# Optimization experiments

Measured on AMD Instinct MI355X. Metric: run time of the kernel, lower is better.

## Reference

```python
import jax, jax.numpy as jnp
import numpy as np

N_HEADS = 16
HEAD_DIM = 128
ROPE_BASE = 50000.0
EPS = 1e-06


def _rotate_half(x):
    half = x.shape[-1] // 2
    return jnp.concatenate([-x[..., half:], x[..., :half]], axis=-1)


def _rms_norm(x, w):
    rms = jnp.sqrt(jnp.mean(x * x, axis=-1, keepdims=True) + EPS)
    return w * (x / rms)


def _rope_tables(n, dim, dtype):
    inv_freq = 1.0 / (ROPE_BASE ** (jnp.arange(0, dim, 2, dtype=jnp.float32) / dim))
    t = jnp.arange(n, dtype=jnp.float32)
    freqs = jnp.outer(t, inv_freq)          # [n, dim/2]
    emb = jnp.concatenate([freqs, freqs], axis=-1)  # [n, dim]
    return jnp.cos(emb).astype(dtype), jnp.sin(emb).astype(dtype)


def setup_inputs() -> dict:
    key = jax.random.key(0)
    ks = jax.random.split(key, 5)
    B, n, d = 2, 2048, 2048
    inner = N_HEADS * HEAD_DIM
    s = 1.0 / np.sqrt(d)
    return {
        "x": jax.random.normal(ks[0], (B, n, d), jnp.float32),
        "Wq": jax.random.normal(ks[1], (d, inner), jnp.float32) * s,
        "Wk": jax.random.normal(ks[2], (d, inner), jnp.float32) * s,
        "Wv": jax.random.normal(ks[3], (d, inner), jnp.float32) * s,
        "Wo": jax.random.normal(ks[4], (inner, d), jnp.float32) * s,
        "qn_w": jnp.ones((inner,), jnp.float32),
        "kn_w": jnp.ones((inner,), jnp.float32),
    }


def reference(x, Wq, Wk, Wv, Wo, qn_w, kn_w):
    B, n, d = x.shape
    # QKV projections (no bias)
    q = x @ Wq
    k = x @ Wk
    v = x @ Wv
    # QK RMSNorm over full inner_dim (as in the torch module)
    q = _rms_norm(q, qn_w)
    k = _rms_norm(k, kn_w)
    # [B, H, n, Dh]
    q = q.reshape(B, n, N_HEADS, HEAD_DIM).transpose(0, 2, 1, 3)
    k = k.reshape(B, n, N_HEADS, HEAD_DIM).transpose(0, 2, 1, 3)
    v = v.reshape(B, n, N_HEADS, HEAD_DIM).transpose(0, 2, 1, 3)
    # RoPE (rotary_dim == head_dim -> full rotation)
    cos, sin = _rope_tables(n, HEAD_DIM, x.dtype)  # [n, Dh]
    cos = cos[None, None]
    sin = sin[None, None]
    q = q * cos + _rotate_half(q) * sin
    k = k * cos + _rotate_half(k) * sin
    # Causal SDPA
    scale = 1.0 / np.sqrt(HEAD_DIM)
    scores = jnp.einsum("bhqd,bhkd->bhqk", q, k) * scale
    causal = jnp.tril(jnp.ones((n, n), dtype=bool))
    scores = jnp.where(causal, scores, jnp.finfo(scores.dtype).min)
    attn = jax.nn.softmax(scores, axis=-1)
    out = jnp.einsum("bhqk,bhkd->bhqd", attn, v)
    out = out.transpose(0, 2, 1, 3).reshape(B, n, N_HEADS * HEAD_DIM)
    return out @ Wo
```

## Files before the change

### kernel.cpp

```cpp
#include <hip/hip_runtime.h>

typedef unsigned short u16;
typedef unsigned int u32;
typedef __attribute__((ext_vector_type(8))) short short8;
typedef __attribute__((ext_vector_type(4))) float f32x4;

typedef __attribute__((address_space(3))) unsigned int as3u32;
typedef __attribute__((address_space(1))) unsigned int as1u32;

__device__ __forceinline__ void gld16(void* lds, const void* g) {
    __builtin_amdgcn_global_load_lds((as1u32*)(void*)g, (as3u32*)lds, 16, 0, 0);
}

__device__ inline float bf2f(u16 u) {
    u32 v = ((u32)u) << 16;
    return __builtin_bit_cast(float, v);
}
__device__ inline u16 f2bf(float f) {
    u32 u = __builtin_bit_cast(u32, f);
    u32 r = u + 0x7FFF + ((u >> 16) & 1);
    return (u16)(r >> 16);
}
__device__ inline void unpack8(uint4 v, float* f) {
    u32 a[4] = {v.x, v.y, v.z, v.w};
#pragma unroll
    for (int i = 0; i < 4; ++i) {
        f[2 * i]     = bf2f((u16)(a[i] & 0xffff));
        f[2 * i + 1] = bf2f((u16)(a[i] >> 16));
    }
}

__global__ __launch_bounds__(256) void cast_f32_bf16(const float* __restrict__ in,
                                                     u16* __restrict__ out, int n) {
    int i = (blockIdx.x * 256 + threadIdx.x) * 4;
    if (i >= n) return;
    float4 v = *(const float4*)&in[i];
    ushort4 o;
    o.x = f2bf(v.x); o.y = f2bf(v.y); o.z = f2bf(v.z); o.w = f2bf(v.w);
    *(ushort4*)&out[i] = o;
}

__global__ __launch_bounds__(256) void transpose_cast(const float* __restrict__ in,
                                                      u16* __restrict__ out, int dim) {
    __shared__ float tile[32][33];
    const int n0 = blockIdx.x * 32, k0 = blockIdx.y * 32;
    const int tx = threadIdx.x & 31, ty = threadIdx.x >> 5;
#pragma unroll
    for (int i = 0; i < 32; i += 8)
        tile[ty + i][tx] = in[(size_t)(k0 + ty + i) * dim + n0 + tx];
    __syncthreads();
#pragma unroll
    for (int i = 0; i < 32; i += 8)
        out[(size_t)(n0 + ty + i) * dim + k0 + tx] = f2bf(tile[tx][ty + i]);
}

__global__ __launch_bounds__(256) void rope_tables(float* __restrict__ cosb,
                                                   float* __restrict__ sinb) {
    int idx = blockIdx.x * 256 + threadIdx.x;
    int pos = idx >> 6, i = idx & 63;
    float invf = __expf(-(float)i * (10.819778284410283f / 64.0f));
    float a = (float)pos * invf;
    cosb[idx] = cosf(a);
    sinb[idx] = sinf(a);
}

template <bool BF16OUT>
__global__ __launch_bounds__(256) void gemm_bt(const u16* __restrict__ A,
                                               const u16* __restrict__ Bt,
                                               void* __restrict__ Cv,
                                               int M, int N, int K) {
    __shared__ u16 As[128][64];
    __shared__ u16 Bs[128][64];
    const int bm = blockIdx.y, bn = blockIdx.x;
    const int tid = threadIdx.x;
    const int lane = tid & 63, w = tid >> 6;
    const int wm = (w >> 1) * 64, wn = (w & 1) * 64;
    const int lrow = lane & 15;
    const int sw = (lane & 7) << 4;
    const int srl = lane >> 3;
    const int ssw = ((lane & 7) * 16) ^ (srl << 4);
    const char* AB = (const char*)A;
    const char* BB = (const char*)Bt;
    f32x4 acc[4][4] = {};

    for (int k0 = 0; k0 < K; k0 += 64) {
        __syncthreads();
#pragma unroll
        for (int i = 0; i < 4; ++i) {
            const int rb = i * 32 + w * 8;
            gld16(&As[rb][0], AB + ((size_t)(bm * 128 + rb + srl) * K + k0) * 2 + ssw);
            gld16(&Bs[rb][0], BB + ((size_t)(bn * 128 + rb + srl) * K + k0) * 2 + ssw);
        }
        __syncthreads();
        const char* AsB = (const char*)As;
        const char* BsB = (const char*)Bs;
#pragma unroll
        for (int kk = 0; kk < 2; ++kk) {
            const int cb = (kk * 64 + (lane >> 4) * 16) ^ sw;
            short8 af[4], bf_[4];
#pragma unroll
            for (int i = 0; i < 4; ++i)
                af[i] = *(const short8*)(AsB + (wm + i * 16 + lrow) * 128 + cb);
#pragma unroll
            for (int j = 0; j < 4; ++j)
                bf_[j] = *(const short8*)(BsB + (wn + j * 16 + lrow) * 128 + cb);
#pragma unroll
            for (int i = 0; i < 4; ++i)
#pragma unroll
                for (int j = 0; j < 4; ++j)
                    acc[i][j] = __builtin_amdgcn_mfma_f32_16x16x32_bf16(af[i], bf_[j], acc[i][j], 0, 0, 0);
        }
    }
    const int crow = (lane >> 4) * 4, ccol = lane & 15;
#pragma unroll
    for (int i = 0; i < 4; ++i)
#pragma unroll
        for (int j = 0; j < 4; ++j)
#pragma unroll
            for (int r = 0; r < 4; ++r) {
                size_t off = (size_t)(bm * 128 + wm + i * 16 + crow + r) * N +
                             (size_t)(bn * 128 + wn + j * 16 + ccol);
                if (BF16OUT) ((u16*)Cv)[off] = f2bf(acc[i][j][r]);
                else         ((float*)Cv)[off] = acc[i][j][r];
            }
}

__global__ __launch_bounds__(256) void norm_rope(const u16* __restrict__ qkv,
                                                 const float* __restrict__ qw,
                                                 const float* __restrict__ kw,
                                                 const float* __restrict__ cosb,
                                                 const float* __restrict__ sinb,
                                                 u16* __restrict__ Qout,
                                                 u16* __restrict__ Kout) {
    __shared__ float qf[2048];
    __shared__ float kf[2048];
    __shared__ float red[8];
    const int r = blockIdx.x;
    const int b = r >> 11, pos = r & 2047;
    const int t = threadIdx.x;
    const u16* row = qkv + (size_t)r * 6144;
    uint4 qv = *(const uint4*)&row[t * 8];
    uint4 kv = *(const uint4*)&row[2048 + t * 8];
    float qe[8], ke[8];
    unpack8(qv, qe);
    unpack8(kv, ke);
    float sq = 0.f, sk = 0.f;
#pragma unroll
    for (int e = 0; e < 8; ++e) {
        qf[t * 8 + e] = qe[e];
        kf[t * 8 + e] = ke[e];
        sq += qe[e] * qe[e];
        sk += ke[e] * ke[e];
    }
#pragma unroll
    for (int msk = 1; msk < 64; msk <<= 1) {
        sq += __shfl_xor(sq, msk);
        sk += __shfl_xor(sk, msk);
    }
    if ((t & 63) == 0) { red[t >> 6] = sq; red[4 + (t >> 6)] = sk; }
    __syncthreads();
    float ssq = red[0] + red[1] + red[2] + red[3];
    float ssk = red[4] + red[5] + red[6] + red[7];
    const float invq = 0.12751946f / sqrtf(ssq * (1.f / 2048.f) + 1e-6f);
    const float invk = 1.0f / sqrtf(ssk * (1.f / 2048.f) + 1e-6f);
    const float* ct = cosb + pos * 64;
    const float* st = sinb + pos * 64;
    u16 qo[8], ko[8];
#pragma unroll
    for (int e = 0; e < 8; ++e) {
        int c = t * 8 + e;
        int jl = c & 127;
        int hb = c & ~127;
        int jj = jl & 63;
        float cs = ct[jj], sn = st[jj];
        int pair = hb + ((jl < 64) ? jl + 64 : jl - 64);
        float sgn = (jl < 64) ? -1.f : 1.f;
        float xq = qf[c] * qw[c], pq = qf[pair] * qw[pair];
        float xk = kf[c] * kw[c], pk = kf[pair] * kw[pair];
        qo[e] = f2bf((xq * cs + sgn * pq * sn) * invq);
        ko[e] = f2bf((xk * cs + sgn * pk * sn) * invk);
    }
    const int h = (t * 8) >> 7;
    const int j0 = (t * 8) & 127;
    size_t o = ((size_t)(b * 16 + h) * 2048 + pos) * 128 + j0;
    *(uint4*)&Qout[o] = *(uint4*)qo;
    *(uint4*)&Kout[o] = *(uint4*)ko;
}

__global__ __launch_bounds__(256) void v_transpose(const u16* __restrict__ qkv,
                                                   u16* __restrict__ Vt) {
    __shared__ u16 tile[64][40];
    const int bxx = blockIdx.x;
    const int jt = bxx & 3, pt = (bxx >> 2) & 31, bh = bxx >> 7;
    const int b = bh >> 4, h = bh & 15;
    const int pos0 = pt * 64, j0 = jt * 32;
    const int t = threadIdx.x;
    {
        int p = t >> 2, jc = (t & 3) * 8;
        const u16* src = qkv + (size_t)(b * 2048 + pos0 + p) * 6144 + 4096 + h * 128 + j0 + jc;
        *(uint4*)&tile[p][jc] = *(const uint4*)src;
    }
    __syncthreads();
    {
        int j = t >> 3, pc = (t & 7) * 8;
        u16 tmp[8];
#pragma unroll
        for (int e = 0; e < 8; ++e) tmp[e] = tile[pc + e][j];
        *(uint4*)&Vt[((size_t)bh * 128 + j0 + j) * 2048 + pos0 + pc] = *(uint4*)tmp;
    }
}

__global__ __launch_bounds__(256) void attn_fwd(const u16* __restrict__ Qr,
                                                const u16* __restrict__ Kr,
                                                const u16* __restrict__ Vt,
                                                u16* __restrict__ O) {
    __shared__ u16 Ks[2][64][128];
    __shared__ u16 Vs[2][128][64];
    __shared__ u16 Pb[4][16][68];
    const int bx = blockIdx.x;
    const int bh = bx >> 4, pi = bx & 15;
    const int tid = threadIdx.x;
    const int lane = tid & 63, w = tid >> 6;
    const int lrow = lane & 15, lk8 = (lane >> 4) * 8;
    const int sw = (lane & 7) << 4;
    const char* KhB = (const char*)(Kr + (size_t)bh * 2048 * 128);
    const char* VhB = (const char*)(Vt + (size_t)bh * 128 * 2048);
    const u16* Qh = Qr + (size_t)bh * 2048 * 128;
    const int b = bh >> 4, h = bh & 15;
    const int krl = lane >> 4;
    const int ksc = (lane & 15) * 16;
    const int vrl = lane >> 3;
    const int vsc = (lane & 7) * 16;

    short8 vone;
#pragma unroll
    for (int i = 0; i < 8; ++i) vone[i] = (short)0x3F80;

    for (int half = 0; half < 2; ++half) {
        const int qt = half ? (31 - pi) : pi;
        const int q0w = qt * 64 + w * 16;
        short8 qa[4];
#pragma unroll
        for (int d = 0; d < 4; ++d)
            qa[d] = *(const short8*)&Qh[(size_t)(q0w + lrow) * 128 + d * 32 + lk8];

        f32x4 acc[9] = {};
        float m[4] = {-3e38f, -3e38f, -3e38f, -3e38f};
        const int rbase = q0w + (lane >> 4) * 4;
        const int kend = qt * 64 + 64;

        __syncthreads();
#pragma unroll
        for (int j = 0; j < 4; ++j) {
            const int krb = w * 16 + j * 4;
            const int kr = krb + krl;
            gld16(&Ks[0][krb][0], KhB + (size_t)kr * 256 + (ksc ^ ((kr & 7) << 4)));
            const int vrb = w * 32 + j * 8;
            const int vr = vrb + vrl;
            gld16(&Vs[0][vrb][0], VhB + (size_t)vr * 4096 + (vsc ^ ((vr & 7) << 4)));
        }

        for (int k0 = 0; k0 < kend; k0 += 64) {
            const int buf = (k0 >> 6) & 1;
            __syncthreads();
            if (k0 + 64 < kend) {
                const int kn = k0 + 64;
#pragma unroll
                for (int j = 0; j < 4; ++j) {
                    const int krb = w * 16 + j * 4;
                    const int kr = krb + krl;
                    gld16(&Ks[buf ^ 1][krb][0],
                          KhB + (size_t)(kn + kr) * 256 + (ksc ^ ((kr & 7) << 4)));
                    const int vrb = w * 32 + j * 8;
                    const int vr = vrb + vrl;
                    gld16(&Vs[buf ^ 1][vrb][0],
                          VhB + (size_t)vr * 4096 + (size_t)kn * 2 + (vsc ^ ((vr & 7) << 4)));
                }
            }
            const char* KsB = (const char*)&Ks[buf][0][0];
            const char* VsB = (const char*)&Vs[buf][0][0];

            f32x4 s[4] = {};
            __builtin_amdgcn_s_setprio(1);
#pragma unroll
            for (int j = 0; j < 4; ++j)
#pragma unroll
                for (int d = 0; d < 4; ++d) {
                    short8 kb = *(const short8*)(KsB + (j * 16 + lrow) * 256 +
                                                 ((d * 64 + (lane >> 4) * 16) ^ sw));
                    s[j] = __builtin_amdgcn_mfma_f32_16x16x32_bf16(qa[d], kb, s[j], 0, 0, 0);
                }
            __builtin_amdgcn_s_setprio(0);

            const bool last = (k0 + 64 >= kend);
            float mx[4];
#pragma unroll
            for (int r = 0; r < 4; ++r) {
                const int rowg = rbase + r;
                if (last) {
#pragma unroll
                    for (int j = 0; j < 4; ++j) {
                        int c = k0 + j * 16 + lrow;
                        s[j][r] = (c <= rowg) ? s[j][r] : -1e30f;
                    }
                }
                float v0 = fmaxf(s[0][r], s[1][r]);
                float v1 = fmaxf(s[2][r], s[3][r]);
                float mr = fmaxf(v0, v1);
#pragma unroll
                for (int msk = 1; msk < 16; msk <<= 1) mr = fmaxf(mr, __shfl_xor(mr, msk));
                mx[r] = mr;
            }
            const bool need = (mx[0] > m[0] + 8.f) | (mx[1] > m[1] + 8.f) |
                              (mx[2] > m[2] + 8.f) | (mx[3] > m[3] + 8.f);
            if (__any(need)) {
                float corr[4];
#pragma unroll
                for (int r = 0; r < 4; ++r) {
                    float mn = fmaxf(m[r], mx[r]);
                    corr[r] = exp2f(m[r] - mn);
                    m[r] = mn;
                }
#pragma unroll
                for (int dt = 0; dt < 9; ++dt) {
                    f32x4 tv = acc[dt];
                    tv[0] *= corr[0]; tv[1] *= corr[1]; tv[2] *= corr[2]; tv[3] *= corr[3];
                    acc[dt] = tv;
                }
            }
#pragma unroll
            for (int r = 0; r < 4; ++r) {
                const int prow = (lane >> 4) * 4 + r;
                Pb[w][prow][0 * 16 + lrow] = f2bf(exp2f(s[0][r] - m[r]));
                Pb[w][prow][1 * 16 + lrow] = f2bf(exp2f(s[1][r] - m[r]));
                Pb[w][prow][2 * 16 + lrow] = f2bf(exp2f(s[2][r] - m[r]));
                Pb[w][prow][3 * 16 + lrow] = f2bf(exp2f(s[3][r] - m[r]));
            }
            short8 pa0 = *(const short8*)&Pb[w][lrow][lk8];
            short8 pa1 = *(const short8*)&Pb[w][lrow][32 + lk8];
            __builtin_amdgcn_s_setprio(1);
            acc[8] = __builtin_amdgcn_mfma_f32_16x16x32_bf16(pa0, vone, acc[8], 0, 0, 0);
            acc[8] = __builtin_amdgcn_mfma_f32_16x16x32_bf16(pa1, vone, acc[8], 0, 0, 0);
#pragma unroll
            for (int dt = 0; dt < 8; ++dt) {
                short8 vb0 = *(const short8*)(VsB + (dt * 16 + lrow) * 128 +
                                              (((lane >> 4) * 16) ^ sw));
                short8 vb1 = *(const short8*)(VsB + (dt * 16 + lrow) * 128 +
                                              ((64 + (lane >> 4) * 16) ^ sw));
                acc[dt] = __builtin_amdgcn_mfma_f32_16x16x32_bf16(pa0, vb0, acc[dt], 0, 0, 0);
                acc[dt] = __builtin_amdgcn_mfma_f32_16x16x32_bf16(pa1, vb1, acc[dt], 0, 0, 0);
            }
            __builtin_amdgcn_s_setprio(0);
        }

#pragma unroll
        for (int r = 0; r < 4; ++r) {
            float inv = 1.0f / acc[8][r];
            int rowg = rbase + r;
            size_t base = ((size_t)b * 2048 + rowg) * 2048 + (size_t)h * 128;
#pragma unroll
            for (int dt = 0; dt < 8; ++dt)
                O[base + dt * 16 + (lane & 15)] = f2bf(acc[dt][r] * inv);
        }
    }
}

extern "C" void kernel_launch(void* const* d_in, const int* in_sizes, int n_in,
                              void* d_out, int out_size, void* d_ws, size_t ws_size,
                              hipStream_t stream) {
    const float* x   = (const float*)d_in[0];
    const float* Wq  = (const float*)d_in[1];
    const float* Wk  = (const float*)d_in[2];
    const float* Wv  = (const float*)d_in[3];
    const float* Wo  = (const float*)d_in[4];
    const float* qnw = (const float*)d_in[5];
    const float* knw = (const float*)d_in[6];

    const size_t MB = 1ull << 20;
    char* ws = (char*)d_ws;
    u16* Xbf    = (u16*)(ws + 0);
    u16* Qr     = (u16*)(ws + 0);
    u16* Wtqkv  = (u16*)(ws + 16 * MB);
    u16* Wot    = (u16*)(ws + 40 * MB);
    u16* QKV    = (u16*)(ws + 48 * MB);
    u16* AOut   = (u16*)(ws + 48 * MB);
    float* cosb = (float*)(ws + 96 * MB);
    float* sinb = (float*)(ws + 96 * MB + 524288);
    u16* Kr     = (u16*)(ws + 97 * MB);
    u16* Vt     = (u16*)(ws + 113 * MB);

    cast_f32_bf16<<<8192, 256, 0, stream>>>(x, Xbf, 4096 * 2048);
    transpose_cast<<<dim3(64, 64), 256, 0, stream>>>(Wq, Wtqkv, 2048);
    transpose_cast<<<dim3(64, 64), 256, 0, stream>>>(Wk, Wtqkv + 2048 * 2048, 2048);
    transpose_cast<<<dim3(64, 64), 256, 0, stream>>>(Wv, Wtqkv + 2 * 2048 * 2048, 2048);
    transpose_cast<<<dim3(64, 64), 256, 0, stream>>>(Wo, Wot, 2048);
    rope_tables<<<512, 256, 0, stream>>>(cosb, sinb);

    gemm_bt<true><<<dim3(48, 32), 256, 0, stream>>>(Xbf, Wtqkv, (void*)QKV, 4096, 6144, 2048);

    norm_rope<<<4096, 256, 0, stream>>>(QKV, qnw, knw, cosb, sinb, Qr, Kr);
    v_transpose<<<4096, 256, 0, stream>>>(QKV, Vt);

    attn_fwd<<<512, 256, 0, stream>>>(Qr, Kr, Vt, AOut);

    gemm_bt<false><<<dim3(16, 32), 256, 0, stream>>>(AOut, Wot, d_out, 4096, 2048, 2048);
}
```

Before: 328.0 us.

## Rewrite attention core with 32x32 MFMA, register-resident P, 128-row query tiles

The attention kernel now computes S^T = K·Q^T with 32x32x16 bf16 MFMAs so each lane owns one query row. The softmax max and sum then need only a single cross-half shuffle, and P is repacked in registers via cvt_pk_bf16 and permlane32_swap instead of going through LDS. Query tiles grow to 128 rows, each wave handles 32 rows, the grid halves to 256 blocks, and blocks are remapped so heads are spread across XCDs. The row sum is now accumulated in scalar form rather than with an extra ones-MFMA. The costs are higher register pressure (launch_bounds 256,1), fewer blocks for load balance, and reliance on gfx950-specific instructions.

Result: faster. 309.4 us (-5.7%).

```diff
diff --git a/kernel.cpp b/kernel.cpp
--- a/kernel.cpp
+++ b/kernel.cpp
@@ -4,6 +4,8 @@
 typedef unsigned int u32;
 typedef __attribute__((ext_vector_type(8))) short short8;
 typedef __attribute__((ext_vector_type(4))) float f32x4;
+typedef __attribute__((ext_vector_type(16))) float f32x16;
+typedef __attribute__((ext_vector_type(4))) u32 u32x4;
 
 typedef __attribute__((address_space(3))) unsigned int as3u32;
 typedef __attribute__((address_space(1))) unsigned int as1u32;
@@ -20,6 +22,11 @@
     u32 u = __builtin_bit_cast(u32, f);
     u32 r = u + 0x7FFF + ((u >> 16) & 1);
     return (u16)(r >> 16);
+}
+__device__ __forceinline__ u32 cvtpk_bf16(float lo, float hi) {
+    u32 r;
+    asm("v_cvt_pk_bf16_f32 %0, %1, %2" : "=v"(r) : "v"(lo), "v"(hi));
+    return r;
 }
 __device__ inline void unpack8(uint4 v, float* f) {
     u32 a[4] = {v.x, v.y, v.z, v.w};
@@ -210,44 +217,41 @@
     }
 }
 
-__global__ __launch_bounds__(256) void attn_fwd(const u16* __restrict__ Qr,
-                                                const u16* __restrict__ Kr,
-                                                const u16* __restrict__ Vt,
-                                                u16* __restrict__ O) {
+__global__ __launch_bounds__(256, 1) void attn_fwd(const u16* __restrict__ Qr,
+                                                   const u16* __restrict__ Kr,
+                                                   const u16* __restrict__ Vt,
+                                                   u16* __restrict__ O) {
     __shared__ u16 Ks[2][64][128];
-    __shared__ u16 Vs[2][128][64];
-    __shared__ u16 Pb[4][16][68];
+    __shared__ u16 VsT[2][128][64];
     const int bx = blockIdx.x;
-    const int bh = bx >> 4, pi = bx & 15;
+    const int xcd = bx & 7, sub = bx >> 3;
+    const int bh = xcd + 8 * (sub & 3);
+    const int pi = sub >> 2;
     const int tid = threadIdx.x;
     const int lane = tid & 63, w = tid >> 6;
-    const int lrow = lane & 15, lk8 = (lane >> 4) * 8;
-    const int sw = (lane & 7) << 4;
+    const int ql = lane & 31, h = lane >> 5;
     const char* KhB = (const char*)(Kr + (size_t)bh * 2048 * 128);
     const char* VhB = (const char*)(Vt + (size_t)bh * 128 * 2048);
     const u16* Qh = Qr + (size_t)bh * 2048 * 128;
-    const int b = bh >> 4, h = bh & 15;
+    const int b = bh >> 4, hh = bh & 15;
     const int krl = lane >> 4;
     const int ksc = (lane & 15) * 16;
     const int vrl = lane >> 3;
     const int vsc = (lane & 7) * 16;
-
-    short8 vone;
-#pragma unroll
-    for (int i = 0; i < 8; ++i) vone[i] = (short)0x3F80;
+    const int swz = (ql & 7) << 4;
 
     for (int half = 0; half < 2; ++half) {
-        const int qt = half ? (31 - pi) : pi;
-        const int q0w = qt * 64 + w * 16;
-        short8 qa[4];
-#pragma unroll
-        for (int d = 0; d < 4; ++d)
-            qa[d] = *(const short8*)&Qh[(size_t)(q0w + lrow) * 128 + d * 32 + lk8];
-
-        f32x4 acc[9] = {};
-        float m[4] = {-3e38f, -3e38f, -3e38f, -3e38f};
-        const int rbase = q0w + (lane >> 4) * 4;
-        const int kend = qt * 64 + 64;
+        const int qt = half ? (15 - pi) : pi;
+        const int q0w = qt * 128 + w * 32;
+        const int qg = q0w + ql;
+        short8 qb[8];
+#pragma unroll
+        for (int s = 0; s < 8; ++s)
+            qb[s] = *(const short8*)&Qh[(size_t)qg * 128 + s * 16 + h * 8];
+
+        f32x16 ot[4] = {};
+        float m = -3e38f, ls = 0.f;
+        const int kend = qt * 128 + 128;
 
         __syncthreads();
 #pragma unroll
@@ -257,7 +261,7 @@
             gld16(&Ks[0][krb][0], KhB + (size_t)kr * 256 + (ksc ^ ((kr & 7) << 4)));
             const int vrb = w * 32 + j * 8;
             const int vr = vrb + vrl;
-            gld16(&Vs[0][vrb][0], VhB + (size_t)vr * 4096 + (vsc ^ ((vr & 7) << 4)));
+            gld16(&VsT[0][vrb][0], VhB + (size_t)vr * 4096 + (vsc ^ ((vr & 7) << 4)));
         }
 
         for (int k0 = 0; k0 < kend; k0 += 64) {
@@ -273,95 +277,102 @@
                           KhB + (size_t)(kn + kr) * 256 + (ksc ^ ((kr & 7) << 4)));
                     const int vrb = w * 32 + j * 8;
                     const int vr = vrb + vrl;
-                    gld16(&Vs[buf ^ 1][vrb][0],
+                    gld16(&VsT[buf ^ 1][vrb][0],
                           VhB + (size_t)vr * 4096 + (size_t)kn * 2 + (vsc ^ ((vr & 7) << 4)));
                 }
             }
             const char* KsB = (const char*)&Ks[buf][0][0];
-            const char* VsB = (const char*)&Vs[buf][0][0];
-
-            f32x4 s[4] = {};
-            __builtin_amdgcn_s_setprio(1);
-#pragma unroll
-            for (int j = 0; j < 4; ++j)
-#pragma unroll
-                for (int d = 0; d < 4; ++d) {
-                    short8 kb = *(const short8*)(KsB + (j * 16 + lrow) * 256 +
-                                                 ((d * 64 + (lane >> 4) * 16) ^ sw));
-                    s[j] = __builtin_amdgcn_mfma_f32_16x16x32_bf16(qa[d], kb, s[j], 0, 0, 0);
+            const char* VsB = (const char*)&VsT[buf][0][0];
+
+            f32x16 st[2] = {};
+#pragma unroll
+            for (int s = 0; s < 8; ++s) {
+                short8 kf0 = *(const short8*)(KsB + (size_t)ql * 256 + ((s * 32 + 16 * h) ^ swz));
+                short8 kf1 = *(const short8*)(KsB + (size_t)(32 + ql) * 256 + ((s * 32 + 16 * h) ^ swz));
+                st[0] = __builtin_amdgcn_mfma_f32_32x32x16_bf16(kf0, qb[s], st[0], 0, 0, 0);
+                st[1] = __builtin_amdgcn_mfma_f32_32x32x16_bf16(kf1, qb[s], st[1], 0, 0, 0);
+            }
+
+            if (k0 + 64 > q0w) {
+#pragma unroll
+                for (int T = 0; T < 2; ++T)
+#pragma unroll
+                    for (int reg = 0; reg < 16; ++reg) {
+                        int c = k0 + 32 * T + (reg & 3) + 8 * (reg >> 2) + 4 * h;
+                        if (c > qg) st[T][reg] = -1e30f;
+                    }
+            }
+
+            float mx = st[0][0];
+#pragma unroll
+            for (int T = 0; T < 2; ++T)
+#pragma unroll
+                for (int reg = 0; reg < 16; ++reg) mx = fmaxf(mx, st[T][reg]);
+            mx = fmaxf(mx, __shfl_xor(mx, 32));
+
+            if (__any(mx > m + 8.f)) {
+                float mn = fmaxf(m, mx);
+                float corr = exp2f(m - mn);
+                m = mn;
+                ls *= corr;
+#pragma unroll
+                for (int td = 0; td < 4; ++td)
+#pragma unroll
+                    for (int reg = 0; reg < 16; ++reg) ot[td][reg] *= corr;
+            }
+
+            float ps = 0.f;
+#pragma unroll
+            for (int T = 0; T < 2; ++T)
+#pragma unroll
+                for (int reg = 0; reg < 16; ++reg) {
+                    float p = exp2f(st[T][reg] - m);
+                    st[T][reg] = p;
+                    ps += p;
                 }
-            __builtin_amdgcn_s_setprio(0);
-
-            const bool last = (k0 + 64 >= kend);
-            float mx[4];
-#pragma unroll
-            for (int r = 0; r < 4; ++r) {
-                const int rowg = rbase + r;
-                if (last) {
-#pragma unroll
-                    for (int j = 0; j < 4; ++j) {
-                        int c = k0 + j * 16 + lrow;
-                        s[j][r] = (c <= rowg) ? s[j][r] : -1e30f;
+            ps += __shfl_xor(ps, 32);
+            ls += ps;
+
+#pragma unroll
+            for (int T = 0; T < 2; ++T) {
+                u32 c[4][2];
+#pragma unroll
+                for (int mm = 0; mm < 4; ++mm) {
+                    c[mm][0] = cvtpk_bf16(st[T][4 * mm + 0], st[T][4 * mm + 1]);
+                    c[mm][1] = cvtpk_bf16(st[T][4 * mm + 2], st[T][4 * mm + 3]);
+                }
+#pragma unroll
+                for (int i = 0; i < 2; ++i) {
+                    const int ks = 2 * T + i;
+                    u32 a0 = c[2 * i][0], b0 = c[2 * i + 1][0];
+                    u32 a1 = c[2 * i][1], b1 = c[2 * i + 1][1];
+                    asm volatile("v_permlane32_swap_b32 %0, %1" : "+v"(a0), "+v"(b0));
+                    asm volatile("v_permlane32_swap_b32 %0, %1" : "+v"(a1), "+v"(b1));
+                    u32x4 pw = {a0, a1, b0, b1};
+                    short8 pf = __builtin_bit_cast(short8, pw);
+#pragma unroll
+                    for (int td = 0; td < 4; ++td) {
+                        short8 vf = *(const short8*)(VsB + (size_t)(32 * td + ql) * 128 +
+                                                     ((32 * ks + 16 * h) ^ swz));
+                        ot[td] = __builtin_amdgcn_mfma_f32_32x32x16_bf16(vf, pf, ot[td], 0, 0, 0);
                     }
                 }
-                float v0 = fmaxf(s[0][r], s[1][r]);
-                float v1 = fmaxf(s[2][r], s[3][r]);
-                float mr = fmaxf(v0, v1);
-#pragma unroll
-                for (int msk = 1; msk < 16; msk <<= 1) mr = fmaxf(mr, __shfl_xor(mr, msk));
-                mx[r] = mr;
-            }
-            const bool need = (mx[0] > m[0] + 8.f) | (mx[1] > m[1] + 8.f) |
-                              (mx[2] > m[2] + 8.f) | (mx[3] > m[3] + 8.f);
-            if (__any(need)) {
-                float corr[4];
-#pragma unroll
-                for (int r = 0; r < 4; ++r) {
-                    float mn = fmaxf(m[r], mx[r]);
-                    corr[r] = exp2f(m[r] - mn);
-                    m[r] = mn;
-                }
-#pragma unroll
-                for (int dt = 0; dt < 9; ++dt) {
-                    f32x4 tv = acc[dt];
-                    tv[0] *= corr[0]; tv[1] *= corr[1]; tv[2] *= corr[2]; tv[3] *= corr[3];
-                    acc[dt] = tv;
-                }
-            }
-#pragma unroll
-            for (int r = 0; r < 4; ++r) {
-                const int prow = (lane >> 4) * 4 + r;
-                Pb[w][prow][0 * 16 + lrow] = f2bf(exp2f(s[0][r] - m[r]));
-                Pb[w][prow][1 * 16 + lrow] = f2bf(exp2f(s[1][r] - m[r]));
-                Pb[w][prow][2 * 16 + lrow] = f2bf(exp2f(s[2][r] - m[r]));
-                Pb[w][prow][3 * 16 + lrow] = f2bf(exp2f(s[3][r] - m[r]));
-            }
-            short8 pa0 = *(const short8*)&Pb[w][lrow][lk8];
-            short8 pa1 = *(const short8*)&Pb[w][lrow][32 + lk8];
-            __builtin_amdgcn_s_setprio(1);
-            acc[8] = __builtin_amdgcn_mfma_f32_16x16x32_bf16(pa0, vone, acc[8], 0, 0, 0);
-            acc[8] = __builtin_amdgcn_mfma_f32_16x16x32_bf16(pa1, vone, acc[8], 0, 0, 0);
-#pragma unroll
-            for (int dt = 0; dt < 8; ++dt) {
-                short8 vb0 = *(const short8*)(VsB + (dt * 16 + lrow) * 128 +
-                                              (((lane >> 4) * 16) ^ sw));
-                short8 vb1 = *(const short8*)(VsB + (dt * 16 + lrow) * 128 +
-                                              ((64 + (lane >> 4) * 16) ^ sw));
-                acc[dt] = __builtin_amdgcn_mfma_f32_16x16x32_bf16(pa0, vb0, acc[dt], 0, 0, 0);
-                acc[dt] = __builtin_amdgcn_mfma_f32_16x16x32_bf16(pa1, vb1, acc[dt], 0, 0, 0);
-            }
-            __builtin_amdgcn_s_setprio(0);
+            }
         }
 
-#pragma unroll
-        for (int r = 0; r < 4; ++r) {
-            float inv = 1.0f / acc[8][r];
-            int rowg = rbase + r;
-            size_t base = ((size_t)b * 2048 + rowg) * 2048 + (size_t)h * 128;
-#pragma unroll
-            for (int dt = 0; dt < 8; ++dt)
-                O[base + dt * 16 + (lane & 15)] = f2bf(acc[dt][r] * inv);
-        }
+        const float inv = 1.0f / ls;
+        const size_t base = ((size_t)b * 2048 + qg) * 2048 + (size_t)hh * 128;
+#pragma unroll
+        for (int td = 0; td < 4; ++td)
+#pragma unroll
+            for (int g = 0; g < 4; ++g) {
+                ushort4 o4;
+                o4.x = f2bf(ot[td][4 * g + 0] * inv);
+                o4.y = f2bf(ot[td][4 * g + 1] * inv);
+                o4.z = f2bf(ot[td][4 * g + 2] * inv);
+                o4.w = f2bf(ot[td][4 * g + 3] * inv);
+                *(ushort4*)&O[base + 32 * td + 8 * g + 4 * h] = o4;
+            }
     }
 }
 
@@ -401,7 +412,7 @@
     norm_rope<<<4096, 256, 0, stream>>>(QKV, qnw, knw, cosb, sinb, Qr, Kr);
     v_transpose<<<4096, 256, 0, stream>>>(QKV, Vt);
 
-    attn_fwd<<<512, 256, 0, stream>>>(Qr, Kr, Vt, AOut);
+    attn_fwd<<<256, 256, 0, stream>>>(Qr, Kr, Vt, AOut);
 
     gemm_bt<false><<<dim3(16, 32), 256, 0, stream>>>(AOut, Wot, d_out, 4096, 2048, 2048);
 }
```
